# Kernel tuning notes

Hardware: AMD Instinct MI355X
Metric: run time of the kernel (lower is better)

Reference implementation:

```python
import jax, jax.numpy as jnp
import numpy as np

B, C, H, W = 8, 64, 64, 64
HID = 256  # hidden width of gate_strength_fc


def _init_params(key):
    ks = jax.random.split(key, 12)
    s = 0.05
    p = {}
    p['Wq'] = jax.random.normal(ks[0], (C, C), jnp.float32) * s
    p['bq'] = jnp.zeros((C,), jnp.float32)
    p['Wk'] = jax.random.normal(ks[1], (C, C), jnp.float32) * s
    p['bk'] = jnp.zeros((C,), jnp.float32)
    p['Wv'] = jax.random.normal(ks[2], (C, C), jnp.float32) * s
    p['bv'] = jnp.zeros((C,), jnp.float32)
    p['Wg'] = jax.random.normal(ks[3], (C, C), jnp.float32) * s
    p['bg'] = jnp.zeros((C,), jnp.float32)
    p['W1'] = jax.random.normal(ks[4], (HID, C), jnp.float32) * s
    p['b1'] = jnp.zeros((HID,), jnp.float32)
    p['W2'] = jax.random.normal(ks[5], (1, HID), jnp.float32) * s
    p['b2'] = jnp.zeros((1,), jnp.float32)
    return p


def setup_inputs() -> dict:
    key = jax.random.key(0)
    k0, k1, k2, kp = jax.random.split(key, 4)
    x = jax.random.normal(k0, (B, C, H, W), jnp.float32)
    # torch.rand(...) > 0.8 dropout-style mask, precomputed as 0/1 float for determinism
    mask = (jax.random.uniform(k1, (B, 1, H, W), jnp.float32) > 0.8).astype(jnp.float32)
    use_entropy_gate = jax.random.bernoulli(k2, 0.5, (B,))
    inp = {'x': x, 'mask': mask, 'use_entropy_gate': use_entropy_gate}
    inp.update(_init_params(kp))
    return inp


def _conv1x1(w, b, t):
    # 1x1 conv == per-pixel matmul over channels
    return jnp.einsum('oc,bchw->bohw', w, t) + b[None, :, None, None]


def reference(x, mask, use_entropy_gate, Wq, bq, Wk, bk, Wv, bv, Wg, bg, W1, b1, W2, b2):
    b_, c_, h_, w_ = x.shape
    n = h_ * w_
    masked_x = x * mask
    q = _conv1x1(Wq, bq, masked_x).reshape(b_, c_, n).transpose(0, 2, 1)  # [B,N,C]
    k = _conv1x1(Wk, bk, masked_x).reshape(b_, c_, n)                      # [B,C,N]
    v = _conv1x1(Wv, bv, x).reshape(b_, c_, n)                             # [B,C,N]
    attn = jax.nn.softmax(jnp.einsum('bnc,bcm->bnm', q, k), axis=-1)       # [B,N,N]
    out = jnp.einsum('bcn,bmn->bcm', v, attn).reshape(b_, c_, h_, w_)
    hidden = jax.nn.relu(_conv1x1(W1, b1, x))
    gate_strength = jax.nn.sigmoid(_conv1x1(W2, b2, hidden))               # [B,1,H,W]
    gate = jax.nn.sigmoid(_conv1x1(Wg, bg, x))                             # [B,C,H,W]
    flag = use_entropy_gate[:, None, None, None]
    return jnp.where(flag, out * gate * gate_strength, x)
```

## Files before the change

### kernel.cpp

```cpp
#include <hip/hip_runtime.h>
#include <hip/hip_bf16.h>
#include <math.h>

namespace {
constexpr int kB = 8;
constexpr int kC = 64;
constexpr int kN = 4096;
constexpr int kCap = 1280;
constexpr int kQS = 1312;
constexpr int kSplit = 4;
constexpr long kSeg = (long)kB * kC * kN;
typedef __attribute__((ext_vector_type(8))) short short8;
typedef __attribute__((ext_vector_type(4))) float f32x4;
}

__global__ __launch_bounds__(256) void dense_kernel(
    const float* __restrict__ x, const float* __restrict__ mask,
    const int* __restrict__ flag,
    const float* __restrict__ Wq, const float* __restrict__ bq,
    const float* __restrict__ Wk, const float* __restrict__ bk,
    const float* __restrict__ Wv, const float* __restrict__ bv,
    const float* __restrict__ Wg, const float* __restrict__ bg,
    const float* __restrict__ W1, const float* __restrict__ b1,
    const float* __restrict__ W2, const float* __restrict__ b2,
    __hip_bfloat16* __restrict__ G, float* __restrict__ GS,
    __hip_bfloat16* __restrict__ Qa, __hip_bfloat16* __restrict__ Ka,
    __hip_bfloat16* __restrict__ VaT, float* __restrict__ Sq,
    float* __restrict__ xmsP, int* __restrict__ p2i, int* __restrict__ cnt) {
  const int b = blockIdx.y;
  if (!flag[b]) return;
  const int tile = blockIdx.x;
  const int n0 = tile * 64;
  const int t = threadIdx.x;
  const int wid = t >> 6;
  const int lane = t & 63;

  __shared__ __hip_bfloat16 sX[64][72];
  __shared__ float sB[512];
  __shared__ float sW2[256];
  __shared__ int sRed[4];
  __shared__ int sI[64];

  {
    const int c = t >> 2;
    const int nn = (t & 3) * 16;
    const float* xp = x + (long)b * kC * kN + (long)c * kN + n0 + nn;
#pragma unroll
    for (int u = 0; u < 16; ++u) sX[nn + u][c] = __float2bfloat16(xp[u]);
  }
  if (t < 64) { sB[t] = bq[t]; sB[64 + t] = bk[t]; sB[128 + t] = bv[t]; sB[192 + t] = bg[t]; }
  sB[256 + t] = b1[t];
  sW2[t] = W2[t];
  int loc = 0;
  for (int n = t; n < n0; n += 256) loc += (mask[b * kN + n] != 0.f) ? 1 : 0;
#pragma unroll
  for (int d = 1; d < 64; d <<= 1) loc += __shfl_xor(loc, d);
  if (lane == 0) sRed[wid] = loc;
  __syncthreads();
  const int pbase = sRed[0] + sRed[1] + sRed[2] + sRed[3];
  if (wid == 0) {
    const bool a = mask[b * kN + n0 + lane] != 0.f;
    const unsigned long long bal = __ballot(a);
    int ia = a ? (pbase + (int)__popcll(bal & ((1ULL << lane) - 1ULL))) : -1;
    if (ia >= kCap) ia = -1;
    sI[lane] = ia;
    p2i[b * kN + n0 + lane] = ia;
    if (tile == 63 && lane == 0) cnt[b] = pbase + (int)__popcll(bal);
  }
  __syncthreads();

  const int col = lane & 15;
  const int quad = lane >> 4;
  const int nl = wid * 16 + col;
  const int n = n0 + nl;
  const short8 bfr0 = *(const short8*)&sX[nl][quad * 8];
  const short8 bfr1 = *(const short8*)&sX[nl][32 + quad * 8];
  const int i_act = sI[nl];
  const float b2v = b2[0];

  float gs_acc = 0.f, sq_acc = 0.f;
  for (int mt = 0; mt < 32; ++mt) {
    const float* Wsrc; int rb0;
    if (mt < 4)       { Wsrc = Wq; rb0 = mt * 16; }
    else if (mt < 8)  { Wsrc = Wk; rb0 = (mt - 4) * 16; }
    else if (mt < 12) { Wsrc = Wv; rb0 = (mt - 8) * 16; }
    else if (mt < 16) { Wsrc = Wg; rb0 = (mt - 12) * 16; }
    else              { Wsrc = W1; rb0 = (mt - 16) * 16; }
    const float* wp = Wsrc + (rb0 + col) * kC + quad * 8;
    short8 a0, a1;
#pragma unroll
    for (int j = 0; j < 8; ++j) {
      ((__hip_bfloat16*)&a0)[j] = __float2bfloat16(wp[j]);
      ((__hip_bfloat16*)&a1)[j] = __float2bfloat16(wp[32 + j]);
    }
    f32x4 acc = {0.f, 0.f, 0.f, 0.f};
    acc = __builtin_amdgcn_mfma_f32_16x16x32_bf16(a0, bfr0, acc, 0, 0, 0);
    acc = __builtin_amdgcn_mfma_f32_16x16x32_bf16(a1, bfr1, acc, 0, 0, 0);
    const int rbase = mt * 16 + quad * 4;
    if (mt < 4) {
      if (i_act >= 0) {
#pragma unroll
        for (int g = 0; g < 4; ++g) {
          const int r = rbase + g;
          const float qv = acc[g] + sB[r];
          Qa[((long)b * kCap + i_act) * kC + r] = __float2bfloat16(qv);
          sq_acc += qv * sB[64 + r];
        }
      }
    } else if (mt < 8) {
      if (i_act >= 0) {
#pragma unroll
        for (int g = 0; g < 4; ++g) {
          const int r = rbase + g;
          Ka[((long)b * kCap + i_act) * kC + (r - 64)] = __float2bfloat16(acc[g] + sB[r]);
        }
      }
    } else if (mt < 12) {
      if (i_act >= 0) {
#pragma unroll
        for (int g = 0; g < 4; ++g) {
          const int r = rbase + g;
          VaT[((long)b * kC + (r - 128)) * kCap + i_act] =
              __float2bfloat16(acc[g] + sB[r]);
        }
      }
    } else if (mt < 16) {
#pragma unroll
      for (int g = 0; g < 4; ++g) {
        const int r = rbase + g;
        const float gv = 1.f / (1.f + __expf(-(acc[g] + sB[r])));
        G[((long)b * kC + (r - 192)) * kN + n] = __float2bfloat16(gv);
      }
    } else {
#pragma unroll
      for (int g = 0; g < 4; ++g) {
        const int r = rbase + g;
        gs_acc += sW2[r - 256] * fmaxf(acc[g] + sB[r], 0.f);
      }
    }
  }
  gs_acc += __shfl_xor(gs_acc, 16);
  gs_acc += __shfl_xor(gs_acc, 32);
  sq_acc += __shfl_xor(sq_acc, 16);
  sq_acc += __shfl_xor(sq_acc, 32);
  if (quad == 0) {
    GS[(long)b * kN + n] = 1.f / (1.f + __expf(-(gs_acc + b2v)));
    if (i_act >= 0) Sq[(long)b * kCap + i_act] = sq_acc;
  }
  {
    const int c = t >> 2;
    const int g4 = t & 3;
    const float* mp = mask + (long)b * kN + n0 + g4 * 16;
    float s = 0.f;
#pragma unroll
    for (int u = 0; u < 16; ++u)
      if (mp[u] == 0.f) s += __bfloat162float(sX[g4 * 16 + u][c]);
    s += __shfl_xor(s, 1);
    s += __shfl_xor(s, 2);
    if (g4 == 0) xmsP[((long)b * 64 + tile) * kC + c] = s;
  }
}

__global__ __launch_bounds__(64) void attn_act_kernel(
    const __hip_bfloat16* __restrict__ Qa, const __hip_bfloat16* __restrict__ Ka,
    const __hip_bfloat16* __restrict__ VaT,
    const int* __restrict__ cnt, const int* __restrict__ flag,
    const float* __restrict__ bq, const float* __restrict__ bk,
    const float* __restrict__ bv, const float* __restrict__ Wv,
    const float* __restrict__ xmsP,
    float* __restrict__ Pm, float* __restrict__ Pl,
    __hip_bfloat16* __restrict__ Po,
    float* __restrict__ Vsum, float* __restrict__ s0M) {
  const int b = blockIdx.z;
  if (!flag[b]) return;
  const int lane = threadIdx.x;

  __shared__ __hip_bfloat16 sP[16][40];
  __shared__ float sxm[kC];

  if (blockIdx.x == kQS / 16) {
    if (blockIdx.y != 0) return;
    float acc = 0.f;
    for (int k = 0; k < 64; ++k) acc += xmsP[((long)b * 64 + k) * kC + lane];
    sxm[lane] = acc;
    __syncthreads();
    float v = 0.f;
#pragma unroll
    for (int o = 0; o < kC; ++o) v += Wv[lane * kC + o] * sxm[o];
    Vsum[b * kC + lane] = v + (float)(kN - cnt[b]) * bv[lane];
    float pp = bq[lane] * bk[lane];
#pragma unroll
    for (int d = 1; d < 64; d <<= 1) pp += __shfl_xor(pp, d);
    if (lane == 0) s0M[0] = pp;
    return;
  }

  const int cc = min(cnt[b], kCap);
  const int ccq = cc + 1;
  const int q0 = blockIdx.x * 16;
  if (q0 >= ccq) return;
  const int s = blockIdx.y;
  const int col = lane & 15;
  const int quad = lane >> 4;
  const int gq = q0 + col;

  const int nT = (cc + 31) >> 5;
  const int tq = (nT + kSplit - 1) / kSplit;
  const int t0 = s * tq;
  const int t1 = min(t0 + tq, nT);
  const long pb = ((long)b * kSplit + s) * kQS + gq;

  if (t0 >= t1) {
    if (gq < ccq) {
      if (quad == 0) { Pm[pb] = -3e38f; Pl[pb] = 0.f; }
#pragma unroll
      for (int ct = 0; ct < 4; ++ct)
#pragma unroll
        for (int g = 0; g < 4; ++g)
          Po[pb * kC + ct * 16 + quad * 4 + g] = __float2bfloat16(0.f);
    }
    return;
  }

  short8 qf0, qf1;
  if (gq == cc) {
#pragma unroll
    for (int j = 0; j < 8; ++j) {
      ((__hip_bfloat16*)&qf0)[j] = __float2bfloat16(bq[quad * 8 + j]);
      ((__hip_bfloat16*)&qf1)[j] = __float2bfloat16(bq[32 + quad * 8 + j]);
    }
  } else {
    const int qrow = (gq < cc) ? gq : (cc - 1);
    const __hip_bfloat16* qr = Qa + ((long)b * kCap + qrow) * kC + quad * 8;
    qf0 = *(const short8*)(qr);
    qf1 = *(const short8*)(qr + 32);
  }

  float Mi = -3e38f, Li = 0.f;
  f32x4 oacc[4];
#pragma unroll
  for (int ct = 0; ct < 4; ++ct) oacc[ct] = (f32x4){0.f, 0.f, 0.f, 0.f};

  for (int kt = t0; kt < t1; ++kt) {
    const int i0 = kt * 32;
    const int kr0 = min(i0 + col, cc - 1);
    const int kr1 = min(i0 + 16 + col, cc - 1);
    const __hip_bfloat16* kp0 = Ka + ((long)b * kCap + kr0) * kC + quad * 8;
    const __hip_bfloat16* kp1 = Ka + ((long)b * kCap + kr1) * kC + quad * 8;
    const short8 kf00 = *(const short8*)(kp0);
    const short8 kf01 = *(const short8*)(kp0 + 32);
    const short8 kf10 = *(const short8*)(kp1);
    const short8 kf11 = *(const short8*)(kp1 + 32);

    f32x4 sa0 = {0.f, 0.f, 0.f, 0.f}, sa1 = {0.f, 0.f, 0.f, 0.f};
    sa0 = __builtin_amdgcn_mfma_f32_16x16x32_bf16(kf00, qf0, sa0, 0, 0, 0);
    sa0 = __builtin_amdgcn_mfma_f32_16x16x32_bf16(kf01, qf1, sa0, 0, 0, 0);
    sa1 = __builtin_amdgcn_mfma_f32_16x16x32_bf16(kf10, qf0, sa1, 0, 0, 0);
    sa1 = __builtin_amdgcn_mfma_f32_16x16x32_bf16(kf11, qf1, sa1, 0, 0, 0);

    float sc[8];
#pragma unroll
    for (int g = 0; g < 4; ++g) {
      sc[g]     = (i0 + quad * 4 + g < cc)      ? sa0[g] : -3e38f;
      sc[4 + g] = (i0 + 16 + quad * 4 + g < cc) ? sa1[g] : -3e38f;
    }
    float lm = sc[0];
#pragma unroll
    for (int u = 1; u < 8; ++u) lm = fmaxf(lm, sc[u]);
    lm = fmaxf(lm, __shfl_xor(lm, 16));
    lm = fmaxf(lm, __shfl_xor(lm, 32));
    const float newM = fmaxf(Mi, lm);
    const float alpha = __expf(Mi - newM);
    float p[8], ps = 0.f;
#pragma unroll
    for (int u = 0; u < 8; ++u) { p[u] = __expf(sc[u] - newM); ps += p[u]; }
    ps += __shfl_xor(ps, 16);
    ps += __shfl_xor(ps, 32);
    Li = Li * alpha + ps;
    Mi = newM;

#pragma unroll
    for (int g = 0; g < 4; ++g) {
      sP[col][quad * 4 + g] = __float2bfloat16(p[g]);
      sP[col][16 + quad * 4 + g] = __float2bfloat16(p[4 + g]);
    }
    __syncthreads();
    const short8 pf = *(const short8*)&sP[col][quad * 8];

#pragma unroll
    for (int ct = 0; ct < 4; ++ct)
#pragma unroll
      for (int g = 0; g < 4; ++g) oacc[ct][g] *= alpha;
#pragma unroll
    for (int ct = 0; ct < 4; ++ct) {
      const short8 vf = *(const short8*)(
          VaT + ((long)b * kC + ct * 16 + col) * kCap + i0 + quad * 8);
      oacc[ct] = __builtin_amdgcn_mfma_f32_16x16x32_bf16(vf, pf, oacc[ct], 0, 0, 0);
    }
    __syncthreads();
  }

  if (gq < ccq) {
    if (quad == 0) { Pm[pb] = Mi; Pl[pb] = Li; }
#pragma unroll
    for (int ct = 0; ct < 4; ++ct)
#pragma unroll
      for (int g = 0; g < 4; ++g)
        Po[pb * kC + ct * 16 + quad * 4 + g] = __float2bfloat16(oacc[ct][g]);
  }
}

__global__ __launch_bounds__(256) void epilogue_kernel(
    const float* __restrict__ x, const int* __restrict__ flag,
    const int* __restrict__ p2i, const int* __restrict__ cnt,
    const float* __restrict__ Pm, const float* __restrict__ Pl,
    const __hip_bfloat16* __restrict__ Po, const float* __restrict__ Sq,
    const float* __restrict__ s0M, const float* __restrict__ Vsum,
    const __hip_bfloat16* __restrict__ G, const float* __restrict__ GS,
    float* __restrict__ out) {
  const int b = blockIdx.z;
  const int cg = blockIdx.y;
  const int n = blockIdx.x * 256 + threadIdx.x;
  const int t = threadIdx.x;
  const long bbase = (long)b * kC * kN + n;
  if (!flag[b]) {
#pragma unroll
    for (int u = 0; u < 16; ++u) {
      const long a = bbase + (long)(cg * 16 + u) * kN;
      out[a] = x[a];
    }
    return;
  }
  const int cTrue = cnt[b];
  const int cc = min(cTrue, kCap);
  const float multF = (float)(kN - cTrue);

  __shared__ float sFac[5];
  __shared__ float sOM16[16];
  __shared__ float sVs[16];
  if (t == 0) {
    const float s0 = s0M[0];
    float mar[kSplit], lar[kSplit];
    float M = s0;
#pragma unroll
    for (int s = 0; s < kSplit; ++s) {
      const long pbs = ((long)b * kSplit + s) * kQS + cc;
      mar[s] = Pm[pbs];
      lar[s] = Pl[pbs];
      M = fmaxf(M, mar[s]);
    }
    const float p0 = __expf(s0 - M);
    float L = multF * p0;
    float wgt[kSplit];
#pragma unroll
    for (int s = 0; s < kSplit; ++s) { wgt[s] = __expf(mar[s] - M); L += lar[s] * wgt[s]; }
    const float invL = 1.f / L;
#pragma unroll
    for (int s = 0; s < kSplit; ++s) sFac[s] = wgt[s] * invL;
    sFac[4] = p0 * invL;
  }
  if (t < 16) sVs[t] = Vsum[b * kC + cg * 16 + t];
  __syncthreads();
  if (t < 16) {
    const int c = cg * 16 + t;
    float o = sFac[4] * sVs[t];
#pragma unroll
    for (int s = 0; s < kSplit; ++s)
      o += sFac[s] * __bfloat162float(Po[(((long)b * kSplit + s) * kQS + cc) * kC + c]);
    sOM16[t] = o;
  }
  __syncthreads();

  const float gsv = GS[(long)b * kN + n];
  const int i = p2i[b * kN + n];
  float fac[kSplit], facP = 0.f;
  if (i >= 0) {
    const float s0 = Sq[(long)b * kCap + i];
    float mar[kSplit], lar[kSplit];
    float M = s0;
#pragma unroll
    for (int s = 0; s < kSplit; ++s) {
      const long pbs = ((long)b * kSplit + s) * kQS + i;
      mar[s] = Pm[pbs];
      lar[s] = Pl[pbs];
      M = fmaxf(M, mar[s]);
    }
    const float p0 = __expf(s0 - M);
    float L = multF * p0;
#pragma unroll
    for (int s = 0; s < kSplit; ++s) { fac[s] = __expf(mar[s] - M); L += lar[s] * fac[s]; }
    const float invL = 1.f / L;
#pragma unroll
    for (int s = 0; s < kSplit; ++s) fac[s] *= invL;
    facP = p0 * invL;
  }
#pragma unroll
  for (int u = 0; u < 16; ++u) {
    const int c = cg * 16 + u;
    float r;
    if (i >= 0) {
      r = facP * sVs[u];
#pragma unroll
      for (int s = 0; s < kSplit; ++s)
        r += fac[s] * __bfloat162float(Po[(((long)b * kSplit + s) * kQS + i) * kC + c]);
    } else {
      r = sOM16[u];
    }
    const long a = bbase + (long)c * kN;
    out[a] = r * __bfloat162float(G[a]) * gsv;
  }
}

extern "C" void kernel_launch(void* const* d_in, const int* in_sizes, int n_in,
                              void* d_out, int out_size, void* d_ws, size_t ws_size,
                              hipStream_t stream) {
  (void)in_sizes; (void)n_in; (void)out_size; (void)ws_size;
  const float* x    = (const float*)d_in[0];
  const float* mask = (const float*)d_in[1];
  const int*   flag = (const int*)d_in[2];
  const float* Wq = (const float*)d_in[3];
  const float* bq = (const float*)d_in[4];
  const float* Wk = (const float*)d_in[5];
  const float* bk = (const float*)d_in[6];
  const float* Wv = (const float*)d_in[7];
  const float* bv = (const float*)d_in[8];
  const float* Wg = (const float*)d_in[9];
  const float* bg = (const float*)d_in[10];
  const float* W1 = (const float*)d_in[11];
  const float* b1 = (const float*)d_in[12];
  const float* W2 = (const float*)d_in[13];
  const float* b2 = (const float*)d_in[14];
  float* out = (float*)d_out;

  char* w = (char*)d_ws;
  float* GS = (float*)w;                       w += (long)kB * kN * 4;
  __hip_bfloat16* G  = (__hip_bfloat16*)w;     w += kSeg * 2;
  __hip_bfloat16* Qa = (__hip_bfloat16*)w;     w += (long)kB * kCap * kC * 2;
  __hip_bfloat16* Ka = (__hip_bfloat16*)w;     w += (long)kB * kCap * kC * 2;
  __hip_bfloat16* VaT= (__hip_bfloat16*)w;     w += (long)kB * kC * kCap * 2;
  __hip_bfloat16* Po = (__hip_bfloat16*)w;     w += (long)kB * kSplit * kQS * kC * 2;
  float* Pm = (float*)w;                       w += (long)kB * kSplit * kQS * 4;
  float* Pl = (float*)w;                       w += (long)kB * kSplit * kQS * 4;
  float* Sq = (float*)w;                       w += (long)kB * kCap * 4;
  float* xmsP = (float*)w;                     w += (long)kB * 64 * kC * 4;
  int* p2i = (int*)w;                          w += (long)kB * kN * 4;
  int* cnt = (int*)w;                          w += 64;
  float* Vsum = (float*)w;                     w += kB * kC * 4;
  float* s0M  = (float*)w;                     w += 64;

  dim3 gd(64, kB);
  dense_kernel<<<gd, 256, 0, stream>>>(x, mask, flag, Wq, bq, Wk, bk, Wv, bv,
                                       Wg, bg, W1, b1, W2, b2,
                                       G, GS, Qa, Ka, VaT, Sq, xmsP, p2i, cnt);
  dim3 gat(kQS / 16 + 1, kSplit, kB);
  attn_act_kernel<<<gat, 64, 0, stream>>>(Qa, Ka, VaT, cnt, flag, bq, bk, bv, Wv,
                                          xmsP, Pm, Pl, Po, Vsum, s0M);
  dim3 gep(kN / 256, 4, kB);
  epilogue_kernel<<<gep, 256, 0, stream>>>(x, flag, p2i, cnt, Pm, Pl, Po, Sq,
                                           s0M, Vsum, G, GS, out);
}
```

Baseline: 144.8 us.

## Stage bf16 weight fragments in LDS, halve attention split, vectorize partial reads

The dense kernel now converts all five weight matrices to bf16 once per block into a 64KB LDS buffer laid out as MFMA A-fragments, replacing per-iteration strided global loads and conversions in the 32-tile loop. The attention split count drops from 4 to 2, which halves the partial-softmax merge work but gives the attention kernel less parallelism. The final combine kernel reads each split's 16-channel partial output as two 16-byte vector loads instead of scalar loads. The large LDS buffer may cut dense-kernel occupancy, and each block repeats the weight staging.

```diff
diff --git a/kernel.cpp b/kernel.cpp
--- a/kernel.cpp
+++ b/kernel.cpp
@@ -8,7 +8,7 @@
 constexpr int kN = 4096;
 constexpr int kCap = 1280;
 constexpr int kQS = 1312;
-constexpr int kSplit = 4;
+constexpr int kSplit = 2;
 constexpr long kSeg = (long)kB * kC * kN;
 typedef __attribute__((ext_vector_type(8))) short short8;
 typedef __attribute__((ext_vector_type(4))) float f32x4;
@@ -35,6 +35,7 @@
   const int wid = t >> 6;
   const int lane = t & 63;
 
+  __shared__ __hip_bfloat16 sWf[4096 * 8];
   __shared__ __hip_bfloat16 sX[64][72];
   __shared__ float sB[512];
   __shared__ float sW2[256];
@@ -51,6 +52,23 @@
   if (t < 64) { sB[t] = bq[t]; sB[64 + t] = bk[t]; sB[128 + t] = bv[t]; sB[192 + t] = bg[t]; }
   sB[256 + t] = b1[t];
   sW2[t] = W2[t];
+  for (int f = t; f < 4096; f += 256) {
+    const int mt = f >> 7;
+    const int ks = (f >> 6) & 1;
+    const int ln = f & 63;
+    const int m = mt * 16 + (ln & 15);
+    const int k0 = ks * 32 + (ln >> 4) * 8;
+    const float* Wsrc;
+    int row;
+    if (m < 64)       { Wsrc = Wq; row = m; }
+    else if (m < 128) { Wsrc = Wk; row = m - 64; }
+    else if (m < 192) { Wsrc = Wv; row = m - 128; }
+    else if (m < 256) { Wsrc = Wg; row = m - 192; }
+    else              { Wsrc = W1; row = m - 256; }
+#pragma unroll
+    for (int j = 0; j < 8; ++j)
+      sWf[f * 8 + j] = __float2bfloat16(Wsrc[row * kC + k0 + j]);
+  }
   int loc = 0;
   for (int n = t; n < n0; n += 256) loc += (mask[b * kN + n] != 0.f) ? 1 : 0;
 #pragma unroll
@@ -78,21 +96,11 @@
   const int i_act = sI[nl];
   const float b2v = b2[0];
 
-  float gs_acc = 0.f, sq_acc = 0.f;
+  float gs_acc = 0.f;
+  float sq_acc = 0.f;
   for (int mt = 0; mt < 32; ++mt) {
-    const float* Wsrc; int rb0;
-    if (mt < 4)       { Wsrc = Wq; rb0 = mt * 16; }
-    else if (mt < 8)  { Wsrc = Wk; rb0 = (mt - 4) * 16; }
-    else if (mt < 12) { Wsrc = Wv; rb0 = (mt - 8) * 16; }
-    else if (mt < 16) { Wsrc = Wg; rb0 = (mt - 12) * 16; }
-    else              { Wsrc = W1; rb0 = (mt - 16) * 16; }
-    const float* wp = Wsrc + (rb0 + col) * kC + quad * 8;
-    short8 a0, a1;
-#pragma unroll
-    for (int j = 0; j < 8; ++j) {
-      ((__hip_bfloat16*)&a0)[j] = __float2bfloat16(wp[j]);
-      ((__hip_bfloat16*)&a1)[j] = __float2bfloat16(wp[32 + j]);
-    }
+    const short8 a0 = *(const short8*)&sWf[((mt * 2 + 0) * 64 + lane) * 8];
+    const short8 a1 = *(const short8*)&sWf[((mt * 2 + 1) * 64 + lane) * 8];
     f32x4 acc = {0.f, 0.f, 0.f, 0.f};
     acc = __builtin_amdgcn_mfma_f32_16x16x32_bf16(a0, bfr0, acc, 0, 0, 0);
     acc = __builtin_amdgcn_mfma_f32_16x16x32_bf16(a1, bfr1, acc, 0, 0, 0);
@@ -335,7 +343,7 @@
   const int cc = min(cTrue, kCap);
   const float multF = (float)(kN - cTrue);
 
-  __shared__ float sFac[5];
+  __shared__ float sFac[kSplit + 1];
   __shared__ float sOM16[16];
   __shared__ float sVs[16];
   if (t == 0) {
@@ -357,13 +365,13 @@
     const float invL = 1.f / L;
 #pragma unroll
     for (int s = 0; s < kSplit; ++s) sFac[s] = wgt[s] * invL;
-    sFac[4] = p0 * invL;
+    sFac[kSplit] = p0 * invL;
   }
   if (t < 16) sVs[t] = Vsum[b * kC + cg * 16 + t];
   __syncthreads();
   if (t < 16) {
     const int c = cg * 16 + t;
-    float o = sFac[4] * sVs[t];
+    float o = sFac[kSplit] * sVs[t];
 #pragma unroll
     for (int s = 0; s < kSplit; ++s)
       o += sFac[s] * __bfloat162float(Po[(((long)b * kSplit + s) * kQS + cc) * kC + c]);
@@ -373,7 +381,7 @@
 
   const float gsv = GS[(long)b * kN + n];
   const int i = p2i[b * kN + n];
-  float fac[kSplit], facP = 0.f;
+  float r16[16];
   if (i >= 0) {
     const float s0 = Sq[(long)b * kCap + i];
     float mar[kSplit], lar[kSplit];
@@ -387,27 +395,34 @@
     }
     const float p0 = __expf(s0 - M);
     float L = multF * p0;
+    float fac[kSplit];
 #pragma unroll
     for (int s = 0; s < kSplit; ++s) { fac[s] = __expf(mar[s] - M); L += lar[s] * fac[s]; }
     const float invL = 1.f / L;
-#pragma unroll
-    for (int s = 0; s < kSplit; ++s) fac[s] *= invL;
-    facP = p0 * invL;
+    const float facP = p0 * invL;
+#pragma unroll
+    for (int u = 0; u < 16; ++u) r16[u] = facP * sVs[u];
+#pragma unroll
+    for (int s = 0; s < kSplit; ++s) {
+      const float f = fac[s] * invL;
+      const __hip_bfloat16* pr =
+          Po + (((long)b * kSplit + s) * kQS + i) * kC + cg * 16;
+      const short8 po0 = *(const short8*)(pr);
+      const short8 po1 = *(const short8*)(pr + 8);
+#pragma unroll
+      for (int u = 0; u < 8; ++u) {
+        r16[u]     += f * __bfloat162float(((const __hip_bfloat16*)&po0)[u]);
+        r16[8 + u] += f * __bfloat162float(((const __hip_bfloat16*)&po1)[u]);
+      }
+    }
+  } else {
+#pragma unroll
+    for (int u = 0; u < 16; ++u) r16[u] = sOM16[u];
   }
 #pragma unroll
   for (int u = 0; u < 16; ++u) {
-    const int c = cg * 16 + u;
-    float r;
-    if (i >= 0) {
-      r = facP * sVs[u];
-#pragma unroll
-      for (int s = 0; s < kSplit; ++s)
-        r += fac[s] * __bfloat162float(Po[(((long)b * kSplit + s) * kQS + i) * kC + c]);
-    } else {
-      r = sOM16[u];
-    }
-    const long a = bbase + (long)c * kN;
-    out[a] = r * __bfloat162float(G[a]) * gsv;
+    const long a = bbase + (long)(cg * 16 + u) * kN;
+    out[a] = r16[u] * __bfloat162float(G[a]) * gsv;
   }
 }
 
```

Result: faster. 122.9 us (median of 2 runs) (-15.2%).
